# Performance work log

Measured on AMD Instinct MI355X. Metric: run time of the kernel, lower is better.

Reference implementation:

```python
import jax, jax.numpy as jnp
import numpy as np

BS, S, D = 2, 2048, 1024
H = 16
DK = D // H  # 64
ROPE_BASE = 10000.0


def _rope(x):
    # x: [b, s, h, dk]; apply rotary embedding along s with per-pair angles.
    s, d = x.shape[1], x.shape[-1]
    theta = 1.0 / (ROPE_BASE ** (jnp.arange(0, d, 2, dtype=jnp.float32) / d))  # [d/2]
    ang = jnp.arange(s, dtype=jnp.float32)[:, None] * theta[None, :]            # [s, d/2]
    cos = jnp.cos(ang)[None, :, None, :]
    sin = jnp.sin(ang)[None, :, None, :]
    xs = x.reshape(*x.shape[:-1], d // 2, 2)
    x0, x1 = xs[..., 0], xs[..., 1]
    out = jnp.stack([x0 * cos - x1 * sin, x1 * cos + x0 * sin], axis=-1)
    return out.reshape(x.shape)


def setup_inputs() -> dict:
    key = jax.random.key(0)
    ks = jax.random.split(key, 7)
    w = 0.02
    return {
        "Q": jax.random.normal(ks[0], (BS, S, D), dtype=jnp.float32),
        "prev": jax.random.normal(ks[1], (BS, H, S, S), dtype=jnp.float32) * 0.1,
        "Wq": jax.random.normal(ks[2], (D, H * DK), dtype=jnp.float32) * w,
        "bq": jnp.zeros((H * DK,), dtype=jnp.float32),
        "Wk": jax.random.normal(ks[3], (D, H * DK), dtype=jnp.float32) * w,
        "bk": jnp.zeros((H * DK,), dtype=jnp.float32),
        "Wv": jax.random.normal(ks[4], (D, H * DK), dtype=jnp.float32) * w,
        "bv": jnp.zeros((H * DK,), dtype=jnp.float32),
        "Wo": jax.random.normal(ks[5], (H * DK, D), dtype=jnp.float32) * w,
        "bo": jnp.zeros((D,), dtype=jnp.float32),
    }


def reference(Q, prev, Wq, bq, Wk, bk, Wv, bv, Wo, bo):
    bs, s, _ = Q.shape
    scale = DK ** -0.5
    # QKV projections (self-attention: K = V = Q)
    q = (Q @ Wq + bq).reshape(bs, s, H, DK)
    k = (Q @ Wk + bk).reshape(bs, s, H, DK)
    v = (Q @ Wv + bv).reshape(bs, s, H, DK)
    # RoPE on q and k (per-call, matching the torch module)
    q = _rope(q)
    k = _rope(k)
    # scores with residual bias from previous layer
    attn_scores = jnp.einsum("bqhd,bkhd->bhqk", q, k) * scale + prev
    attn_weights = jax.nn.softmax(attn_scores, axis=-1)  # dropout p=0.0
    out = jnp.einsum("bhqk,bkhd->bqhd", attn_weights, v).reshape(bs, s, H * DK)
    out = out @ Wo + bo  # proj dropout p=0.0
    return out, attn_scores
```

## Files before the change

### kernel.cpp

```cpp
#include <hip/hip_runtime.h>
#include <hip/hip_bf16.h>
#include <math.h>

#define S_LEN 2048
#define D_MODEL 1024
#define NH 16
#define DKH 64
#define BSZ 2

typedef __attribute__((ext_vector_type(8))) short s16x8;
typedef __attribute__((ext_vector_type(4))) float f32x4;

__device__ __forceinline__ unsigned short f2bf(float f) {
  unsigned int u = __float_as_uint(f);
  return (unsigned short)((u + 0x7fffu + ((u >> 16) & 1u)) >> 16);
}

__global__ void k_rope_table(float* __restrict__ cosT, float* __restrict__ sinT) {
  int idx = blockIdx.x * 256 + threadIdx.x;
  if (idx >= S_LEN * 32) return;
  int s = idx >> 5, i = idx & 31;
  float theta = powf(10000.0f, -(float)i / 32.0f);
  float ang = (float)s * theta;
  float sv, cv;
  sincosf(ang, &sv, &cv);
  cosT[idx] = cv;
  sinT[idx] = sv;
}

__global__ __launch_bounds__(256) void k_wtrans(const float* __restrict__ W,
                                                unsigned short* __restrict__ WT) {
  __shared__ float t[32][33];
  int n0 = blockIdx.x * 32, k0 = blockIdx.y * 32;
  int tx = threadIdx.x & 31, ty = threadIdx.x >> 5;
#pragma unroll
  for (int p = 0; p < 4; ++p)
    t[ty + p * 8][tx] = W[(size_t)(k0 + ty + p * 8) * 1024 + n0 + tx];
  __syncthreads();
#pragma unroll
  for (int p = 0; p < 4; ++p)
    WT[(size_t)(n0 + ty + p * 8) * 1024 + k0 + tx] = f2bf(t[tx][ty + p * 8]);
}

__global__ __launch_bounds__(256) void k_vtrans(const unsigned short* __restrict__ vl,
                                                unsigned short* __restrict__ vt) {
  __shared__ unsigned short t[64][65];
  int bh = blockIdx.y;
  int s0 = blockIdx.x * 64;
  int tx = threadIdx.x & 3;
  int r = threadIdx.x >> 2;
  const unsigned short* src = vl + (size_t)bh * S_LEN * DKH + (size_t)s0 * DKH;
  s16x8 a = *(const s16x8*)(src + r * 64 + tx * 16);
  s16x8 b = *(const s16x8*)(src + r * 64 + tx * 16 + 8);
#pragma unroll
  for (int j = 0; j < 8; ++j) { t[r][tx * 16 + j] = (unsigned short)a[j]; t[r][tx * 16 + 8 + j] = (unsigned short)b[j]; }
  __syncthreads();
  unsigned short* dst = vt + (size_t)bh * DKH * S_LEN + (size_t)r * S_LEN + s0;
  s16x8 o0, o1;
#pragma unroll
  for (int j = 0; j < 8; ++j) { o0[j] = (short)t[tx * 16 + j][r]; o1[j] = (short)t[tx * 16 + 8 + j][r]; }
  *(s16x8*)(dst + tx * 16) = o0;
  *(s16x8*)(dst + tx * 16 + 8) = o1;
}

__global__ __launch_bounds__(256) void k_qkv(
    const float* __restrict__ Q, const unsigned short* __restrict__ WTqkv,
    const float* __restrict__ bq, const float* __restrict__ bk, const float* __restrict__ bv,
    const float* __restrict__ cosT, const float* __restrict__ sinT,
    unsigned short* __restrict__ ql, unsigned short* __restrict__ kl,
    unsigned short* __restrict__ vl) {
  __shared__ unsigned short As[128][72];
  __shared__ unsigned short Bs[128][72];
  const int m0 = blockIdx.y * 128;
  const int n0 = blockIdx.x * 128;
  const int tid = threadIdx.x;
  const int lane = tid & 63, wave = tid >> 6;
  const int wm = (wave >> 1) * 64, wn = (wave & 1) * 64;
  const int lr = lane & 15, lg = lane >> 4;
  const int widx = n0 >> 10;
  const float* bias = widx == 0 ? bq : (widx == 1 ? bk : bv);

  f32x4 acc[4][4] = {};
  const int arow = tid >> 1, ahalf = tid & 1;

  for (int k0 = 0; k0 < 1024; k0 += 64) {
    __syncthreads();
    {
      const float* src = Q + (size_t)(m0 + arow) * 1024 + k0 + ahalf * 32;
      unsigned short* dstp = &As[arow][ahalf * 32];
#pragma unroll
      for (int j = 0; j < 4; ++j) {
        float4 v0 = ((const float4*)src)[2 * j];
        float4 v1 = ((const float4*)src)[2 * j + 1];
        s16x8 o;
        o[0] = (short)f2bf(v0.x); o[1] = (short)f2bf(v0.y); o[2] = (short)f2bf(v0.z); o[3] = (short)f2bf(v0.w);
        o[4] = (short)f2bf(v1.x); o[5] = (short)f2bf(v1.y); o[6] = (short)f2bf(v1.z); o[7] = (short)f2bf(v1.w);
        *(s16x8*)(dstp + j * 8) = o;
      }
      const s16x8* bsrc = (const s16x8*)(WTqkv + (size_t)(n0 + arow) * 1024 + k0 + ahalf * 32);
      unsigned short* bdst = &Bs[arow][ahalf * 32];
#pragma unroll
      for (int j = 0; j < 4; ++j) *(s16x8*)(bdst + j * 8) = bsrc[j];
    }
    __syncthreads();
#pragma unroll
    for (int ks = 0; ks < 2; ++ks) {
      s16x8 af[4], bf[4];
#pragma unroll
      for (int i = 0; i < 4; ++i) af[i] = *(const s16x8*)&As[wm + i * 16 + lr][ks * 32 + lg * 8];
#pragma unroll
      for (int i = 0; i < 4; ++i) bf[i] = *(const s16x8*)&Bs[wn + i * 16 + lr][ks * 32 + lg * 8];
#pragma unroll
      for (int mi = 0; mi < 4; ++mi)
#pragma unroll
        for (int ni = 0; ni < 4; ++ni)
          acc[mi][ni] = __builtin_amdgcn_mfma_f32_16x16x32_bf16(af[mi], bf[ni], acc[mi][ni], 0, 0, 0);
    }
  }

#pragma unroll
  for (int ni = 0; ni < 4; ++ni) {
    int n = n0 + wn + ni * 16 + lr;
    int np = n & 1023;
    float bval = bias[np];
    int h = np >> 6, d = np & 63;
    int ia = d >> 1;
#pragma unroll
    for (int mi = 0; mi < 4; ++mi) {
#pragma unroll
      for (int r = 0; r < 4; ++r) {
        int m = m0 + wm + mi * 16 + lg * 4 + r;
        int s = m & 2047, b = m >> 11;
        float val = acc[mi][ni][r] + bval;
        size_t oidx = ((size_t)(b * 16 + h) * 2048 + s) * 64 + d;
        if (widx == 2) {
          vl[oidx] = f2bf(val);
        } else {
          float part = __shfl_xor(val, 1);
          float c = cosT[s * 32 + ia], sn = sinT[s * 32 + ia];
          float outv = (d & 1) ? (val * c + part * sn) : (val * c - part * sn);
          (widx == 0 ? ql : kl)[oidx] = f2bf(outv);
        }
      }
    }
  }
}

__global__ __launch_bounds__(256) void k_attn(
    const unsigned short* __restrict__ ql, const unsigned short* __restrict__ kl,
    const unsigned short* __restrict__ vt, const float* __restrict__ prev,
    float* __restrict__ scores, unsigned short* __restrict__ attn_out) {
  __shared__ unsigned short Ks[128][72];
  __shared__ unsigned short Vs[64][136];
  __shared__ unsigned short Ps[4][16][136];
  const int bh = blockIdx.y;
  const int q0 = blockIdx.x * 64;
  const int tid = threadIdx.x, lane = tid & 63, wave = tid >> 6;
  const int lr = lane & 15, lg = lane >> 4;
  const int qw = q0 + wave * 16;

  s16x8 qf[2];
#pragma unroll
  for (int ks = 0; ks < 2; ++ks)
    qf[ks] = *(const s16x8*)(ql + ((size_t)bh * 2048 + qw + lr) * 64 + ks * 32 + lg * 8);

  f32x4 o[4] = {};
  float m_run[4], l_run[4];
#pragma unroll
  for (int r = 0; r < 4; ++r) { m_run[r] = -1e30f; l_run[r] = 0.f; }

  const float scale = 0.125f;
  const float* prevB = prev + (size_t)bh * S_LEN * S_LEN;
  float* scoB = scores + (size_t)bh * S_LEN * S_LEN;

  const int sr = tid >> 1, shf = tid & 1;
  const int dv = tid >> 2, q4 = tid & 3;

  for (int kv0 = 0; kv0 < 2048; kv0 += 128) {
    __syncthreads();
    {
      const s16x8* ksrc = (const s16x8*)(kl + ((size_t)bh * 2048 + kv0 + sr) * 64 + shf * 32);
#pragma unroll
      for (int j = 0; j < 4; ++j) *(s16x8*)&Ks[sr][shf * 32 + j * 8] = ksrc[j];
      const s16x8* vsrc = (const s16x8*)(vt + (size_t)bh * DKH * S_LEN + (size_t)dv * S_LEN + kv0 + q4 * 32);
#pragma unroll
      for (int j = 0; j < 4; ++j) *(s16x8*)&Vs[dv][q4 * 32 + j * 8] = vsrc[j];
    }
    __syncthreads();

    f32x4 sc[8];
#pragma unroll
    for (int n = 0; n < 8; ++n) {
      f32x4 a = {};
#pragma unroll
      for (int ks = 0; ks < 2; ++ks) {
        s16x8 kf = *(const s16x8*)&Ks[n * 16 + lr][ks * 32 + lg * 8];
        a = __builtin_amdgcn_mfma_f32_16x16x32_bf16(qf[ks], kf, a, 0, 0, 0);
      }
      sc[n] = a;
    }

    float tmax[4] = {-1e30f, -1e30f, -1e30f, -1e30f};
#pragma unroll
    for (int n = 0; n < 8; ++n) {
      int col = kv0 + n * 16 + lr;
#pragma unroll
      for (int r = 0; r < 4; ++r) {
        int row = qw + lg * 4 + r;
        float v = sc[n][r] * scale + prevB[(size_t)row * S_LEN + col];
        scoB[(size_t)row * S_LEN + col] = v;
        sc[n][r] = v;
        tmax[r] = fmaxf(tmax[r], v);
      }
    }
#pragma unroll
    for (int mask = 1; mask < 16; mask <<= 1)
#pragma unroll
      for (int r = 0; r < 4; ++r) tmax[r] = fmaxf(tmax[r], __shfl_xor(tmax[r], mask));

    float al[4];
#pragma unroll
    for (int r = 0; r < 4; ++r) {
      float mn = fmaxf(m_run[r], tmax[r]);
      al[r] = __expf(m_run[r] - mn);
      m_run[r] = mn;
      l_run[r] *= al[r];
    }
#pragma unroll
    for (int df = 0; df < 4; ++df)
#pragma unroll
      for (int r = 0; r < 4; ++r) o[df][r] *= al[r];

#pragma unroll
    for (int n = 0; n < 8; ++n) {
#pragma unroll
      for (int r = 0; r < 4; ++r) {
        float p = __expf(sc[n][r] - m_run[r]);
        l_run[r] += p;
        Ps[wave][lg * 4 + r][n * 16 + lr] = f2bf(p);
      }
    }
    __syncthreads();

#pragma unroll
    for (int df = 0; df < 4; ++df) {
#pragma unroll
      for (int ks = 0; ks < 4; ++ks) {
        s16x8 pa = *(const s16x8*)&Ps[wave][lr][ks * 32 + lg * 8];
        s16x8 vb = *(const s16x8*)&Vs[df * 16 + lr][ks * 32 + lg * 8];
        o[df] = __builtin_amdgcn_mfma_f32_16x16x32_bf16(pa, vb, o[df], 0, 0, 0);
      }
    }
  }

#pragma unroll
  for (int mask = 1; mask < 16; mask <<= 1)
#pragma unroll
    for (int r = 0; r < 4; ++r) l_run[r] += __shfl_xor(l_run[r], mask);
  float inv[4];
#pragma unroll
  for (int r = 0; r < 4; ++r) inv[r] = 1.0f / l_run[r];

  int b = bh >> 4, h = bh & 15;
#pragma unroll
  for (int df = 0; df < 4; ++df) {
    int d = df * 16 + lr;
#pragma unroll
    for (int r = 0; r < 4; ++r) {
      int row = qw + lg * 4 + r;
      attn_out[((size_t)(b * 2048 + row)) * 1024 + h * 64 + d] = f2bf(o[df][r] * inv[r]);
    }
  }
}

__global__ __launch_bounds__(256) void k_outproj(
    const unsigned short* __restrict__ A, const unsigned short* __restrict__ WoT,
    const float* __restrict__ bo, float* __restrict__ out) {
  __shared__ unsigned short As[128][72];
  __shared__ unsigned short Bs[128][72];
  const int m0 = blockIdx.y * 128, n0 = blockIdx.x * 128;
  const int tid = threadIdx.x, lane = tid & 63, wave = tid >> 6;
  const int wm = (wave >> 1) * 64, wn = (wave & 1) * 64;
  const int lr = lane & 15, lg = lane >> 4;
  f32x4 acc[4][4] = {};
  const int r = tid >> 1, hfl = tid & 1;
  for (int k0 = 0; k0 < 1024; k0 += 64) {
    __syncthreads();
    const s16x8* asrc = (const s16x8*)(A + (size_t)(m0 + r) * 1024 + k0 + hfl * 32);
    const s16x8* bsrc = (const s16x8*)(WoT + (size_t)(n0 + r) * 1024 + k0 + hfl * 32);
#pragma unroll
    for (int j = 0; j < 4; ++j) {
      *(s16x8*)&As[r][hfl * 32 + j * 8] = asrc[j];
      *(s16x8*)&Bs[r][hfl * 32 + j * 8] = bsrc[j];
    }
    __syncthreads();
#pragma unroll
    for (int ks = 0; ks < 2; ++ks) {
      s16x8 af[4], bf[4];
#pragma unroll
      for (int i = 0; i < 4; ++i) af[i] = *(const s16x8*)&As[wm + i * 16 + lr][ks * 32 + lg * 8];
#pragma unroll
      for (int i = 0; i < 4; ++i) bf[i] = *(const s16x8*)&Bs[wn + i * 16 + lr][ks * 32 + lg * 8];
#pragma unroll
      for (int mi = 0; mi < 4; ++mi)
#pragma unroll
        for (int ni = 0; ni < 4; ++ni)
          acc[mi][ni] = __builtin_amdgcn_mfma_f32_16x16x32_bf16(af[mi], bf[ni], acc[mi][ni], 0, 0, 0);
    }
  }
#pragma unroll
  for (int ni = 0; ni < 4; ++ni) {
    int n = n0 + wn + ni * 16 + lr;
    float bv = bo[n];
#pragma unroll
    for (int mi = 0; mi < 4; ++mi)
#pragma unroll
      for (int rr = 0; rr < 4; ++rr) {
        int m = m0 + wm + mi * 16 + lg * 4 + rr;
        out[(size_t)m * 1024 + n] = acc[mi][ni][rr] + bv;
      }
  }
}

extern "C" void kernel_launch(void* const* d_in, const int* in_sizes, int n_in,
                              void* d_out, int out_size, void* d_ws, size_t ws_size,
                              hipStream_t stream) {
  const float* Q = (const float*)d_in[0];
  const float* prev = (const float*)d_in[1];
  const float* Wq = (const float*)d_in[2];
  const float* bq = (const float*)d_in[3];
  const float* Wk = (const float*)d_in[4];
  const float* bk = (const float*)d_in[5];
  const float* Wv = (const float*)d_in[6];
  const float* bv = (const float*)d_in[7];
  const float* Wo = (const float*)d_in[8];
  const float* bo = (const float*)d_in[9];

  float* out = (float*)d_out;
  float* scores = out + (size_t)4194304;

  char* ws = (char*)d_ws;
  float* cosT = (float*)ws;
  float* sinT = cosT + 65536;
  unsigned short* WTqkv = (unsigned short*)(ws + 524288);
  unsigned short* WoT = WTqkv + 3145728;
  unsigned short* ql = WoT + 1048576;
  unsigned short* kl = ql + 4194304;
  unsigned short* vl = kl + 4194304;
  unsigned short* vt = vl + 4194304;
  unsigned short* attn_out = vt + 4194304;

  k_rope_table<<<256, 256, 0, stream>>>(cosT, sinT);
  k_wtrans<<<dim3(32, 32), 256, 0, stream>>>(Wq, WTqkv);
  k_wtrans<<<dim3(32, 32), 256, 0, stream>>>(Wk, WTqkv + 1048576);
  k_wtrans<<<dim3(32, 32), 256, 0, stream>>>(Wv, WTqkv + 2097152);
  k_wtrans<<<dim3(32, 32), 256, 0, stream>>>(Wo, WoT);
  k_qkv<<<dim3(24, 32), 256, 0, stream>>>(Q, WTqkv, bq, bk, bv, cosT, sinT, ql, kl, vl);
  k_vtrans<<<dim3(32, 32), 256, 0, stream>>>(vl, vt);
  k_attn<<<dim3(32, 32), 256, 0, stream>>>(ql, kl, vt, prev, scores, attn_out);
  k_outproj<<<dim3(8, 32), 256, 0, stream>>>(attn_out, WoT, bo, out);
}
```

Baseline: 410.1 us.

## Rewrite attention with 32x32 MFMA register-resident P and direct global-to-LDS GEMM loads

The attention kernel now computes scores transposed (K as the A operand) with 32x32x16 MFMA. It keeps P in registers via lane shuffles instead of a shared-memory round trip, reads K and V directly from global memory without LDS staging, and uses nontemporal vector loads and stores for prev and scores. The grid is remapped to 512 blocks of 128 queries with launch bounds of 2. The QKV and output projection GEMMs switch to global_load_lds 16-byte async copies into unpadded LDS tiles, and Q is pre-converted to bf16 in a separate kernel. The aim is to cut LDS traffic and syncs and to stream the large fp32 prev/scores arrays efficiently. The risks are more LDS bank conflicts in the unpadded layouts and uncached repeated global reads of K and V.

```diff
diff --git a/kernel.cpp b/kernel.cpp
--- a/kernel.cpp
+++ b/kernel.cpp
@@ -1,19 +1,28 @@
 #include <hip/hip_runtime.h>
 #include <hip/hip_bf16.h>
 #include <math.h>
+#include <cstdint>
 
 #define S_LEN 2048
-#define D_MODEL 1024
-#define NH 16
 #define DKH 64
-#define BSZ 2
 
 typedef __attribute__((ext_vector_type(8))) short s16x8;
+typedef __attribute__((ext_vector_type(4))) short s16x4;
 typedef __attribute__((ext_vector_type(4))) float f32x4;
+typedef __attribute__((ext_vector_type(16))) float f32x16;
 
 __device__ __forceinline__ unsigned short f2bf(float f) {
   unsigned int u = __float_as_uint(f);
   return (unsigned short)((u + 0x7fffu + ((u >> 16) & 1u)) >> 16);
+}
+__device__ __forceinline__ unsigned int pack2bf(float a, float b) {
+  return (unsigned int)f2bf(a) | ((unsigned int)f2bf(b) << 16);
+}
+
+__device__ __forceinline__ void glds16(const unsigned short* g, unsigned short* l) {
+  __builtin_amdgcn_global_load_lds(
+      (const __attribute__((address_space(1))) unsigned int*)(uintptr_t)g,
+      (__attribute__((address_space(3))) unsigned int*)(uintptr_t)l, 16, 0, 0);
 }
 
 __global__ void k_rope_table(float* __restrict__ cosT, float* __restrict__ sinT) {
@@ -42,6 +51,17 @@
     WT[(size_t)(n0 + ty + p * 8) * 1024 + k0 + tx] = f2bf(t[tx][ty + p * 8]);
 }
 
+__global__ __launch_bounds__(256) void k_qconv(const float* __restrict__ Q,
+                                               unsigned short* __restrict__ Qbf) {
+  int idx = (blockIdx.x * 256 + threadIdx.x) * 8;
+  float4 a = *(const float4*)(Q + idx);
+  float4 b = *(const float4*)(Q + idx + 4);
+  s16x8 o;
+  o[0] = (short)f2bf(a.x); o[1] = (short)f2bf(a.y); o[2] = (short)f2bf(a.z); o[3] = (short)f2bf(a.w);
+  o[4] = (short)f2bf(b.x); o[5] = (short)f2bf(b.y); o[6] = (short)f2bf(b.z); o[7] = (short)f2bf(b.w);
+  *(s16x8*)(Qbf + idx) = o;
+}
+
 __global__ __launch_bounds__(256) void k_vtrans(const unsigned short* __restrict__ vl,
                                                 unsigned short* __restrict__ vt) {
   __shared__ unsigned short t[64][65];
@@ -64,52 +84,38 @@
 }
 
 __global__ __launch_bounds__(256) void k_qkv(
-    const float* __restrict__ Q, const unsigned short* __restrict__ WTqkv,
+    const unsigned short* __restrict__ Qbf, const unsigned short* __restrict__ WTqkv,
     const float* __restrict__ bq, const float* __restrict__ bk, const float* __restrict__ bv,
     const float* __restrict__ cosT, const float* __restrict__ sinT,
     unsigned short* __restrict__ ql, unsigned short* __restrict__ kl,
     unsigned short* __restrict__ vl) {
-  __shared__ unsigned short As[128][72];
-  __shared__ unsigned short Bs[128][72];
-  const int m0 = blockIdx.y * 128;
-  const int n0 = blockIdx.x * 128;
-  const int tid = threadIdx.x;
-  const int lane = tid & 63, wave = tid >> 6;
+  __shared__ unsigned short As[128 * 64];
+  __shared__ unsigned short Bs[128 * 64];
+  const int m0 = blockIdx.y * 128, n0 = blockIdx.x * 128;
+  const int tid = threadIdx.x, lane = tid & 63, wave = tid >> 6;
   const int wm = (wave >> 1) * 64, wn = (wave & 1) * 64;
   const int lr = lane & 15, lg = lane >> 4;
   const int widx = n0 >> 10;
   const float* bias = widx == 0 ? bq : (widx == 1 ? bk : bv);
+  const int lrow = lane >> 3, lcol = (lane & 7) * 8;
 
   f32x4 acc[4][4] = {};
-  const int arow = tid >> 1, ahalf = tid & 1;
-
   for (int k0 = 0; k0 < 1024; k0 += 64) {
     __syncthreads();
-    {
-      const float* src = Q + (size_t)(m0 + arow) * 1024 + k0 + ahalf * 32;
-      unsigned short* dstp = &As[arow][ahalf * 32];
-#pragma unroll
-      for (int j = 0; j < 4; ++j) {
-        float4 v0 = ((const float4*)src)[2 * j];
-        float4 v1 = ((const float4*)src)[2 * j + 1];
-        s16x8 o;
-        o[0] = (short)f2bf(v0.x); o[1] = (short)f2bf(v0.y); o[2] = (short)f2bf(v0.z); o[3] = (short)f2bf(v0.w);
-        o[4] = (short)f2bf(v1.x); o[5] = (short)f2bf(v1.y); o[6] = (short)f2bf(v1.z); o[7] = (short)f2bf(v1.w);
-        *(s16x8*)(dstp + j * 8) = o;
-      }
-      const s16x8* bsrc = (const s16x8*)(WTqkv + (size_t)(n0 + arow) * 1024 + k0 + ahalf * 32);
-      unsigned short* bdst = &Bs[arow][ahalf * 32];
-#pragma unroll
-      for (int j = 0; j < 4; ++j) *(s16x8*)(bdst + j * 8) = bsrc[j];
+#pragma unroll
+    for (int i = 0; i < 4; ++i) {
+      int chunk = wave * 4 + i;
+      glds16(Qbf + (size_t)(m0 + 8 * chunk + lrow) * 1024 + k0 + lcol, &As[chunk * 512]);
+      glds16(WTqkv + (size_t)(n0 + 8 * chunk + lrow) * 1024 + k0 + lcol, &Bs[chunk * 512]);
     }
     __syncthreads();
 #pragma unroll
     for (int ks = 0; ks < 2; ++ks) {
       s16x8 af[4], bf[4];
 #pragma unroll
-      for (int i = 0; i < 4; ++i) af[i] = *(const s16x8*)&As[wm + i * 16 + lr][ks * 32 + lg * 8];
-#pragma unroll
-      for (int i = 0; i < 4; ++i) bf[i] = *(const s16x8*)&Bs[wn + i * 16 + lr][ks * 32 + lg * 8];
+      for (int i = 0; i < 4; ++i) af[i] = *(const s16x8*)&As[(wm + i * 16 + lr) * 64 + ks * 32 + lg * 8];
+#pragma unroll
+      for (int i = 0; i < 4; ++i) bf[i] = *(const s16x8*)&Bs[(wn + i * 16 + lr) * 64 + ks * 32 + lg * 8];
 #pragma unroll
       for (int mi = 0; mi < 4; ++mi)
 #pragma unroll
@@ -146,161 +152,167 @@
   }
 }
 
-__global__ __launch_bounds__(256) void k_attn(
+__global__ __launch_bounds__(256, 2) void k_attn(
     const unsigned short* __restrict__ ql, const unsigned short* __restrict__ kl,
     const unsigned short* __restrict__ vt, const float* __restrict__ prev,
     float* __restrict__ scores, unsigned short* __restrict__ attn_out) {
-  __shared__ unsigned short Ks[128][72];
-  __shared__ unsigned short Vs[64][136];
-  __shared__ unsigned short Ps[4][16][136];
-  const int bh = blockIdx.y;
-  const int q0 = blockIdx.x * 64;
+  int wg = blockIdx.x;
+  int c = wg >> 3, r = wg & 7;
+  int bh = r * 4 + (c >> 4);
+  int q0 = (c & 15) * 128;
   const int tid = threadIdx.x, lane = tid & 63, wave = tid >> 6;
-  const int lr = lane & 15, lg = lane >> 4;
-  const int qw = q0 + wave * 16;
-
-  s16x8 qf[2];
-#pragma unroll
-  for (int ks = 0; ks < 2; ++ks)
-    qf[ks] = *(const s16x8*)(ql + ((size_t)bh * 2048 + qw + lr) * 64 + ks * 32 + lg * 8);
-
-  f32x4 o[4] = {};
-  float m_run[4], l_run[4];
-#pragma unroll
-  for (int r = 0; r < 4; ++r) { m_run[r] = -1e30f; l_run[r] = 0.f; }
-
+  const int h = lane >> 5, qcol = lane & 31;
+  const int q = q0 + wave * 32 + qcol;
+
+  const unsigned short* qrow = ql + ((size_t)bh * S_LEN + q) * DKH;
+  s16x8 qf[4];
+#pragma unroll
+  for (int dk = 0; dk < 4; ++dk) qf[dk] = *(const s16x8*)(qrow + dk * 16 + h * 8);
+
+  f32x16 o[2] = {};
+  float m_run = -1e30f, l_run = 0.f;
   const float scale = 0.125f;
-  const float* prevB = prev + (size_t)bh * S_LEN * S_LEN;
-  float* scoB = scores + (size_t)bh * S_LEN * S_LEN;
-
-  const int sr = tid >> 1, shf = tid & 1;
-  const int dv = tid >> 2, q4 = tid & 3;
-
-  for (int kv0 = 0; kv0 < 2048; kv0 += 128) {
-    __syncthreads();
-    {
-      const s16x8* ksrc = (const s16x8*)(kl + ((size_t)bh * 2048 + kv0 + sr) * 64 + shf * 32);
-#pragma unroll
-      for (int j = 0; j < 4; ++j) *(s16x8*)&Ks[sr][shf * 32 + j * 8] = ksrc[j];
-      const s16x8* vsrc = (const s16x8*)(vt + (size_t)bh * DKH * S_LEN + (size_t)dv * S_LEN + kv0 + q4 * 32);
-#pragma unroll
-      for (int j = 0; j < 4; ++j) *(s16x8*)&Vs[dv][q4 * 32 + j * 8] = vsrc[j];
-    }
-    __syncthreads();
-
-    f32x4 sc[8];
-#pragma unroll
-    for (int n = 0; n < 8; ++n) {
-      f32x4 a = {};
-#pragma unroll
-      for (int ks = 0; ks < 2; ++ks) {
-        s16x8 kf = *(const s16x8*)&Ks[n * 16 + lr][ks * 32 + lg * 8];
-        a = __builtin_amdgcn_mfma_f32_16x16x32_bf16(qf[ks], kf, a, 0, 0, 0);
-      }
-      sc[n] = a;
-    }
-
-    float tmax[4] = {-1e30f, -1e30f, -1e30f, -1e30f};
-#pragma unroll
-    for (int n = 0; n < 8; ++n) {
-      int col = kv0 + n * 16 + lr;
-#pragma unroll
-      for (int r = 0; r < 4; ++r) {
-        int row = qw + lg * 4 + r;
-        float v = sc[n][r] * scale + prevB[(size_t)row * S_LEN + col];
-        scoB[(size_t)row * S_LEN + col] = v;
-        sc[n][r] = v;
-        tmax[r] = fmaxf(tmax[r], v);
-      }
-    }
-#pragma unroll
-    for (int mask = 1; mask < 16; mask <<= 1)
-#pragma unroll
-      for (int r = 0; r < 4; ++r) tmax[r] = fmaxf(tmax[r], __shfl_xor(tmax[r], mask));
-
-    float al[4];
-#pragma unroll
-    for (int r = 0; r < 4; ++r) {
-      float mn = fmaxf(m_run[r], tmax[r]);
-      al[r] = __expf(m_run[r] - mn);
-      m_run[r] = mn;
-      l_run[r] *= al[r];
-    }
-#pragma unroll
-    for (int df = 0; df < 4; ++df)
-#pragma unroll
-      for (int r = 0; r < 4; ++r) o[df][r] *= al[r];
-
-#pragma unroll
-    for (int n = 0; n < 8; ++n) {
-#pragma unroll
-      for (int r = 0; r < 4; ++r) {
-        float p = __expf(sc[n][r] - m_run[r]);
-        l_run[r] += p;
-        Ps[wave][lg * 4 + r][n * 16 + lr] = f2bf(p);
-      }
-    }
-    __syncthreads();
-
-#pragma unroll
-    for (int df = 0; df < 4; ++df) {
-#pragma unroll
-      for (int ks = 0; ks < 4; ++ks) {
-        s16x8 pa = *(const s16x8*)&Ps[wave][lr][ks * 32 + lg * 8];
-        s16x8 vb = *(const s16x8*)&Vs[df * 16 + lr][ks * 32 + lg * 8];
-        o[df] = __builtin_amdgcn_mfma_f32_16x16x32_bf16(pa, vb, o[df], 0, 0, 0);
-      }
-    }
-  }
-
-#pragma unroll
-  for (int mask = 1; mask < 16; mask <<= 1)
-#pragma unroll
-    for (int r = 0; r < 4; ++r) l_run[r] += __shfl_xor(l_run[r], mask);
-  float inv[4];
-#pragma unroll
-  for (int r = 0; r < 4; ++r) inv[r] = 1.0f / l_run[r];
-
-  int b = bh >> 4, h = bh & 15;
-#pragma unroll
-  for (int df = 0; df < 4; ++df) {
-    int d = df * 16 + lr;
-#pragma unroll
-    for (int r = 0; r < 4; ++r) {
-      int row = qw + lg * 4 + r;
-      attn_out[((size_t)(b * 2048 + row)) * 1024 + h * 64 + d] = f2bf(o[df][r] * inv[r]);
-    }
-  }
+  const float* prevR = prev + (size_t)bh * S_LEN * S_LEN + (size_t)q * S_LEN;
+  float* scoR = scores + (size_t)bh * S_LEN * S_LEN + (size_t)q * S_LEN;
+  const unsigned short* kbase = kl + (size_t)bh * S_LEN * DKH;
+  const unsigned short* vbase = vt + (size_t)bh * DKH * S_LEN + (size_t)qcol * S_LEN;
+
+  for (int kv0 = 0; kv0 < S_LEN; kv0 += 128) {
+    f32x16 sc[4];
+#pragma unroll
+    for (int t = 0; t < 4; ++t) {
+      const unsigned short* krow = kbase + (size_t)(kv0 + t * 32 + qcol) * DKH + h * 8;
+      f32x16 a = {};
+#pragma unroll
+      for (int dk = 0; dk < 4; ++dk) {
+        s16x8 kf = *(const s16x8*)(krow + dk * 16);
+        a = __builtin_amdgcn_mfma_f32_32x32x16_bf16(kf, qf[dk], a, 0, 0, 0);
+      }
+      sc[t] = a;
+    }
+    float tmax = -1e30f;
+#pragma unroll
+    for (int t = 0; t < 4; ++t) {
+#pragma unroll
+      for (int j = 0; j < 4; ++j) {
+        int kvo = kv0 + t * 32 + 8 * j + 4 * h;
+        f32x4 pv = __builtin_nontemporal_load((const f32x4*)(prevR + kvo));
+        f32x4 sv;
+        sv[0] = sc[t][4 * j + 0] * scale + pv[0];
+        sv[1] = sc[t][4 * j + 1] * scale + pv[1];
+        sv[2] = sc[t][4 * j + 2] * scale + pv[2];
+        sv[3] = sc[t][4 * j + 3] * scale + pv[3];
+        __builtin_nontemporal_store(sv, (f32x4*)(scoR + kvo));
+        sc[t][4 * j + 0] = sv[0]; sc[t][4 * j + 1] = sv[1];
+        sc[t][4 * j + 2] = sv[2]; sc[t][4 * j + 3] = sv[3];
+        tmax = fmaxf(tmax, fmaxf(fmaxf(sv[0], sv[1]), fmaxf(sv[2], sv[3])));
+      }
+    }
+    tmax = fmaxf(tmax, __shfl_xor(tmax, 32));
+    float mn = fmaxf(m_run, tmax);
+    float al = __expf(m_run - mn);
+    m_run = mn;
+    float lsum = 0.f;
+#pragma unroll
+    for (int t = 0; t < 4; ++t)
+#pragma unroll
+      for (int e = 0; e < 16; ++e) {
+        float p = __expf(sc[t][e] - mn);
+        sc[t][e] = p;
+        lsum += p;
+      }
+    l_run = l_run * al + (lsum + __shfl_xor(lsum, 32));
+#pragma unroll
+    for (int dt = 0; dt < 2; ++dt)
+#pragma unroll
+      for (int e = 0; e < 16; ++e) o[dt][e] *= al;
+
+    s16x8 pb[8];
+#pragma unroll
+    for (int g = 0; g < 4; ++g) {
+      unsigned int qu[4][2];
+#pragma unroll
+      for (int j = 0; j < 4; ++j) {
+        qu[j][0] = pack2bf(sc[g][4 * j + 0], sc[g][4 * j + 1]);
+        qu[j][1] = pack2bf(sc[g][4 * j + 2], sc[g][4 * j + 3]);
+      }
+      {
+        unsigned int s0 = h ? qu[0][0] : qu[1][0];
+        unsigned int s1 = h ? qu[0][1] : qu[1][1];
+        unsigned int r0 = __shfl_xor(s0, 32);
+        unsigned int r1 = __shfl_xor(s1, 32);
+        union { s16x8 v; unsigned int u[4]; } fa;
+        fa.u[0] = h ? r0 : qu[0][0];
+        fa.u[1] = h ? r1 : qu[0][1];
+        fa.u[2] = h ? qu[1][0] : r0;
+        fa.u[3] = h ? qu[1][1] : r1;
+        pb[2 * g] = fa.v;
+      }
+      {
+        unsigned int s0 = h ? qu[2][0] : qu[3][0];
+        unsigned int s1 = h ? qu[2][1] : qu[3][1];
+        unsigned int r0 = __shfl_xor(s0, 32);
+        unsigned int r1 = __shfl_xor(s1, 32);
+        union { s16x8 v; unsigned int u[4]; } fb;
+        fb.u[0] = h ? r0 : qu[2][0];
+        fb.u[1] = h ? r1 : qu[2][1];
+        fb.u[2] = h ? qu[3][0] : r0;
+        fb.u[3] = h ? qu[3][1] : r1;
+        pb[2 * g + 1] = fb.v;
+      }
+    }
+#pragma unroll
+    for (int kt = 0; kt < 8; ++kt) {
+      const unsigned short* vrow = vbase + kv0 + kt * 16 + h * 8;
+#pragma unroll
+      for (int dt = 0; dt < 2; ++dt) {
+        s16x8 vf = *(const s16x8*)(vrow + (size_t)dt * 32 * S_LEN);
+        o[dt] = __builtin_amdgcn_mfma_f32_32x32x16_bf16(vf, pb[kt], o[dt], 0, 0, 0);
+      }
+    }
+  }
+
+  float inv = 1.0f / l_run;
+  int b = bh >> 4, hh = bh & 15;
+  unsigned short* orow = attn_out + ((size_t)(b * S_LEN + q)) * 1024 + hh * 64;
+#pragma unroll
+  for (int dt = 0; dt < 2; ++dt)
+#pragma unroll
+    for (int jj = 0; jj < 4; ++jj) {
+      s16x4 ov;
+#pragma unroll
+      for (int i = 0; i < 4; ++i) ov[i] = (short)f2bf(o[dt][4 * jj + i] * inv);
+      *(s16x4*)(orow + dt * 32 + 8 * jj + 4 * h) = ov;
+    }
 }
 
 __global__ __launch_bounds__(256) void k_outproj(
     const unsigned short* __restrict__ A, const unsigned short* __restrict__ WoT,
     const float* __restrict__ bo, float* __restrict__ out) {
-  __shared__ unsigned short As[128][72];
-  __shared__ unsigned short Bs[128][72];
+  __shared__ unsigned short As[128 * 64];
+  __shared__ unsigned short Bs[128 * 64];
   const int m0 = blockIdx.y * 128, n0 = blockIdx.x * 128;
   const int tid = threadIdx.x, lane = tid & 63, wave = tid >> 6;
   const int wm = (wave >> 1) * 64, wn = (wave & 1) * 64;
   const int lr = lane & 15, lg = lane >> 4;
+  const int lrow = lane >> 3, lcol = (lane & 7) * 8;
   f32x4 acc[4][4] = {};
-  const int r = tid >> 1, hfl = tid & 1;
   for (int k0 = 0; k0 < 1024; k0 += 64) {
     __syncthreads();
-    const s16x8* asrc = (const s16x8*)(A + (size_t)(m0 + r) * 1024 + k0 + hfl * 32);
-    const s16x8* bsrc = (const s16x8*)(WoT + (size_t)(n0 + r) * 1024 + k0 + hfl * 32);
-#pragma unroll
-    for (int j = 0; j < 4; ++j) {
-      *(s16x8*)&As[r][hfl * 32 + j * 8] = asrc[j];
-      *(s16x8*)&Bs[r][hfl * 32 + j * 8] = bsrc[j];
+#pragma unroll
+    for (int i = 0; i < 4; ++i) {
+      int chunk = wave * 4 + i;
+      glds16(A + (size_t)(m0 + 8 * chunk + lrow) * 1024 + k0 + lcol, &As[chunk * 512]);
+      glds16(WoT + (size_t)(n0 + 8 * chunk + lrow) * 1024 + k0 + lcol, &Bs[chunk * 512]);
     }
     __syncthreads();
 #pragma unroll
     for (int ks = 0; ks < 2; ++ks) {
       s16x8 af[4], bf[4];
 #pragma unroll
-      for (int i = 0; i < 4; ++i) af[i] = *(const s16x8*)&As[wm + i * 16 + lr][ks * 32 + lg * 8];
-#pragma unroll
-      for (int i = 0; i < 4; ++i) bf[i] = *(const s16x8*)&Bs[wn + i * 16 + lr][ks * 32 + lg * 8];
+      for (int i = 0; i < 4; ++i) af[i] = *(const s16x8*)&As[(wm + i * 16 + lr) * 64 + ks * 32 + lg * 8];
+#pragma unroll
+      for (int i = 0; i < 4; ++i) bf[i] = *(const s16x8*)&Bs[(wn + i * 16 + lr) * 64 + ks * 32 + lg * 8];
 #pragma unroll
       for (int mi = 0; mi < 4; ++mi)
 #pragma unroll
@@ -349,14 +361,16 @@
   unsigned short* vl = kl + 4194304;
   unsigned short* vt = vl + 4194304;
   unsigned short* attn_out = vt + 4194304;
+  unsigned short* Qbf = attn_out + 4194304;
 
   k_rope_table<<<256, 256, 0, stream>>>(cosT, sinT);
   k_wtrans<<<dim3(32, 32), 256, 0, stream>>>(Wq, WTqkv);
   k_wtrans<<<dim3(32, 32), 256, 0, stream>>>(Wk, WTqkv + 1048576);
   k_wtrans<<<dim3(32, 32), 256, 0, stream>>>(Wv, WTqkv + 2097152);
   k_wtrans<<<dim3(32, 32), 256, 0, stream>>>(Wo, WoT);
-  k_qkv<<<dim3(24, 32), 256, 0, stream>>>(Q, WTqkv, bq, bk, bv, cosT, sinT, ql, kl, vl);
+  k_qconv<<<2048, 256, 0, stream>>>(Q, Qbf);
+  k_qkv<<<dim3(24, 32), 256, 0, stream>>>(Qbf, WTqkv, bq, bk, bv, cosT, sinT, ql, kl, vl);
   k_vtrans<<<dim3(32, 32), 256, 0, stream>>>(vl, vt);
-  k_attn<<<dim3(32, 32), 256, 0, stream>>>(ql, kl, vt, prev, scores, attn_out);
+  k_attn<<<512, 256, 0, stream>>>(ql, kl, vt, prev, scores, attn_out);
   k_outproj<<<dim3(8, 32), 256, 0, stream>>>(attn_out, WoT, bo, out);
 }
```

New measurement: 716.4 us. 74.7% more time.

## Use direct global-to-LDS loads, XOR swizzles, bigger attention blocks and XCD-aware mapping

Applied to the files above, without the earlier changes.

Replaces register-staged shared-memory fills in the QKV, attention and output GEMMs with global_load_lds direct copies. This requires a separate kernel that converts Q to bf16 first. The attention kernel moves to 512-thread blocks covering 128 queries, remaps block IDs so heads cluster per XCD, and XOR-swizzles the unpadded K/V/P tiles to avoid bank conflicts. It also drops the barrier before the P·V step, since each wave now uses its own P buffer, and uses nontemporal loads and stores for the large prev/scores streams. The goal is to cut load-issue overhead and cache pollution, at the cost of an extra conversion pass over Q.

```diff
diff --git a/kernel.cpp b/kernel.cpp
--- a/kernel.cpp
+++ b/kernel.cpp
@@ -1,12 +1,10 @@
 #include <hip/hip_runtime.h>
 #include <hip/hip_bf16.h>
 #include <math.h>
+#include <cstdint>
 
 #define S_LEN 2048
-#define D_MODEL 1024
-#define NH 16
 #define DKH 64
-#define BSZ 2
 
 typedef __attribute__((ext_vector_type(8))) short s16x8;
 typedef __attribute__((ext_vector_type(4))) float f32x4;
@@ -14,6 +12,12 @@
 __device__ __forceinline__ unsigned short f2bf(float f) {
   unsigned int u = __float_as_uint(f);
   return (unsigned short)((u + 0x7fffu + ((u >> 16) & 1u)) >> 16);
+}
+
+__device__ __forceinline__ void glds16(const unsigned short* g, unsigned short* l) {
+  __builtin_amdgcn_global_load_lds(
+      (const __attribute__((address_space(1))) unsigned int*)(uintptr_t)g,
+      (__attribute__((address_space(3))) unsigned int*)(uintptr_t)l, 16, 0, 0);
 }
 
 __global__ void k_rope_table(float* __restrict__ cosT, float* __restrict__ sinT) {
@@ -42,6 +46,17 @@
     WT[(size_t)(n0 + ty + p * 8) * 1024 + k0 + tx] = f2bf(t[tx][ty + p * 8]);
 }
 
+__global__ __launch_bounds__(256) void k_qconv(const float* __restrict__ Q,
+                                               unsigned short* __restrict__ Qbf) {
+  int idx = (blockIdx.x * 256 + threadIdx.x) * 8;
+  float4 a = *(const float4*)(Q + idx);
+  float4 b = *(const float4*)(Q + idx + 4);
+  s16x8 o;
+  o[0] = (short)f2bf(a.x); o[1] = (short)f2bf(a.y); o[2] = (short)f2bf(a.z); o[3] = (short)f2bf(a.w);
+  o[4] = (short)f2bf(b.x); o[5] = (short)f2bf(b.y); o[6] = (short)f2bf(b.z); o[7] = (short)f2bf(b.w);
+  *(s16x8*)(Qbf + idx) = o;
+}
+
 __global__ __launch_bounds__(256) void k_vtrans(const unsigned short* __restrict__ vl,
                                                 unsigned short* __restrict__ vt) {
   __shared__ unsigned short t[64][65];
@@ -64,52 +79,38 @@
 }
 
 __global__ __launch_bounds__(256) void k_qkv(
-    const float* __restrict__ Q, const unsigned short* __restrict__ WTqkv,
+    const unsigned short* __restrict__ Qbf, const unsigned short* __restrict__ WTqkv,
     const float* __restrict__ bq, const float* __restrict__ bk, const float* __restrict__ bv,
     const float* __restrict__ cosT, const float* __restrict__ sinT,
     unsigned short* __restrict__ ql, unsigned short* __restrict__ kl,
     unsigned short* __restrict__ vl) {
-  __shared__ unsigned short As[128][72];
-  __shared__ unsigned short Bs[128][72];
-  const int m0 = blockIdx.y * 128;
-  const int n0 = blockIdx.x * 128;
-  const int tid = threadIdx.x;
-  const int lane = tid & 63, wave = tid >> 6;
+  __shared__ unsigned short As[128 * 64];
+  __shared__ unsigned short Bs[128 * 64];
+  const int m0 = blockIdx.y * 128, n0 = blockIdx.x * 128;
+  const int tid = threadIdx.x, lane = tid & 63, wave = tid >> 6;
   const int wm = (wave >> 1) * 64, wn = (wave & 1) * 64;
   const int lr = lane & 15, lg = lane >> 4;
   const int widx = n0 >> 10;
   const float* bias = widx == 0 ? bq : (widx == 1 ? bk : bv);
+  const int lrow = lane >> 3, lcol = (lane & 7) * 8;
 
   f32x4 acc[4][4] = {};
-  const int arow = tid >> 1, ahalf = tid & 1;
-
   for (int k0 = 0; k0 < 1024; k0 += 64) {
     __syncthreads();
-    {
-      const float* src = Q + (size_t)(m0 + arow) * 1024 + k0 + ahalf * 32;
-      unsigned short* dstp = &As[arow][ahalf * 32];
-#pragma unroll
-      for (int j = 0; j < 4; ++j) {
-        float4 v0 = ((const float4*)src)[2 * j];
-        float4 v1 = ((const float4*)src)[2 * j + 1];
-        s16x8 o;
-        o[0] = (short)f2bf(v0.x); o[1] = (short)f2bf(v0.y); o[2] = (short)f2bf(v0.z); o[3] = (short)f2bf(v0.w);
-        o[4] = (short)f2bf(v1.x); o[5] = (short)f2bf(v1.y); o[6] = (short)f2bf(v1.z); o[7] = (short)f2bf(v1.w);
-        *(s16x8*)(dstp + j * 8) = o;
-      }
-      const s16x8* bsrc = (const s16x8*)(WTqkv + (size_t)(n0 + arow) * 1024 + k0 + ahalf * 32);
-      unsigned short* bdst = &Bs[arow][ahalf * 32];
-#pragma unroll
-      for (int j = 0; j < 4; ++j) *(s16x8*)(bdst + j * 8) = bsrc[j];
+#pragma unroll
+    for (int i = 0; i < 4; ++i) {
+      int chunk = wave * 4 + i;
+      glds16(Qbf + (size_t)(m0 + 8 * chunk + lrow) * 1024 + k0 + lcol, &As[chunk * 512]);
+      glds16(WTqkv + (size_t)(n0 + 8 * chunk + lrow) * 1024 + k0 + lcol, &Bs[chunk * 512]);
     }
     __syncthreads();
 #pragma unroll
     for (int ks = 0; ks < 2; ++ks) {
       s16x8 af[4], bf[4];
 #pragma unroll
-      for (int i = 0; i < 4; ++i) af[i] = *(const s16x8*)&As[wm + i * 16 + lr][ks * 32 + lg * 8];
-#pragma unroll
-      for (int i = 0; i < 4; ++i) bf[i] = *(const s16x8*)&Bs[wn + i * 16 + lr][ks * 32 + lg * 8];
+      for (int i = 0; i < 4; ++i) af[i] = *(const s16x8*)&As[(wm + i * 16 + lr) * 64 + ks * 32 + lg * 8];
+#pragma unroll
+      for (int i = 0; i < 4; ++i) bf[i] = *(const s16x8*)&Bs[(wn + i * 16 + lr) * 64 + ks * 32 + lg * 8];
 #pragma unroll
       for (int mi = 0; mi < 4; ++mi)
 #pragma unroll
@@ -146,23 +147,27 @@
   }
 }
 
-__global__ __launch_bounds__(256) void k_attn(
+__global__ __launch_bounds__(512, 4) void k_attn(
     const unsigned short* __restrict__ ql, const unsigned short* __restrict__ kl,
     const unsigned short* __restrict__ vt, const float* __restrict__ prev,
     float* __restrict__ scores, unsigned short* __restrict__ attn_out) {
-  __shared__ unsigned short Ks[128][72];
-  __shared__ unsigned short Vs[64][136];
-  __shared__ unsigned short Ps[4][16][136];
-  const int bh = blockIdx.y;
-  const int q0 = blockIdx.x * 64;
+  __shared__ unsigned short Ks[128 * 64];
+  __shared__ unsigned short Vs[64 * 128];
+  __shared__ unsigned short Ps[8 * 16 * 128];
+
+  int bid = blockIdx.x;
+  int xcd = bid & 7, idx = bid >> 3;
+  int bh = xcd * 4 + (idx >> 4);
+  int qb = idx & 15;
+
   const int tid = threadIdx.x, lane = tid & 63, wave = tid >> 6;
   const int lr = lane & 15, lg = lane >> 4;
-  const int qw = q0 + wave * 16;
+  const int qw = qb * 128 + wave * 16;
 
   s16x8 qf[2];
 #pragma unroll
   for (int ks = 0; ks < 2; ++ks)
-    qf[ks] = *(const s16x8*)(ql + ((size_t)bh * 2048 + qw + lr) * 64 + ks * 32 + lg * 8);
+    qf[ks] = *(const s16x8*)(ql + ((size_t)bh * S_LEN + qw + lr) * DKH + ks * 32 + lg * 8);
 
   f32x4 o[4] = {};
   float m_run[4], l_run[4];
@@ -170,21 +175,28 @@
   for (int r = 0; r < 4; ++r) { m_run[r] = -1e30f; l_run[r] = 0.f; }
 
   const float scale = 0.125f;
+  const unsigned short* kbase = kl + (size_t)bh * S_LEN * DKH;
+  const unsigned short* vbase = vt + (size_t)bh * DKH * S_LEN;
   const float* prevB = prev + (size_t)bh * S_LEN * S_LEN;
   float* scoB = scores + (size_t)bh * S_LEN * S_LEN;
-
-  const int sr = tid >> 1, shf = tid & 1;
-  const int dv = tid >> 2, q4 = tid & 3;
-
-  for (int kv0 = 0; kv0 < 2048; kv0 += 128) {
-    __syncthreads();
-    {
-      const s16x8* ksrc = (const s16x8*)(kl + ((size_t)bh * 2048 + kv0 + sr) * 64 + shf * 32);
-#pragma unroll
-      for (int j = 0; j < 4; ++j) *(s16x8*)&Ks[sr][shf * 32 + j * 8] = ksrc[j];
-      const s16x8* vsrc = (const s16x8*)(vt + (size_t)bh * DKH * S_LEN + (size_t)dv * S_LEN + kv0 + q4 * 32);
-#pragma unroll
-      for (int j = 0; j < 4; ++j) *(s16x8*)&Vs[dv][q4 * 32 + j * 8] = vsrc[j];
+  unsigned short* PsW = &Ps[wave * 2048];
+
+  const int kr = lane >> 3, kc = lane & 7;
+  const int vr = lane >> 4, vc = lane & 15;
+
+  for (int kv0 = 0; kv0 < S_LEN; kv0 += 128) {
+    __syncthreads();
+#pragma unroll
+    for (int half = 0; half < 2; ++half) {
+      int rbase = half * 64 + wave * 8;
+      int row = rbase + kr;
+      glds16(kbase + (size_t)(kv0 + row) * DKH + ((kc ^ (row & 7)) * 8), &Ks[rbase * 64]);
+    }
+#pragma unroll
+    for (int half = 0; half < 2; ++half) {
+      int dbase = wave * 8 + half * 4;
+      int d = dbase + vr;
+      glds16(vbase + (size_t)d * S_LEN + kv0 + ((vc ^ (d & 7)) * 8), &Vs[dbase * 128]);
     }
     __syncthreads();
 
@@ -194,7 +206,9 @@
       f32x4 a = {};
 #pragma unroll
       for (int ks = 0; ks < 2; ++ks) {
-        s16x8 kf = *(const s16x8*)&Ks[n * 16 + lr][ks * 32 + lg * 8];
+        int row = n * 16 + lr;
+        s16x8 kf = *(const s16x8*)((const char*)Ks +
+                                   row * 128 + ((ks * 64 + lg * 16) ^ ((lr & 7) << 4)));
         a = __builtin_amdgcn_mfma_f32_16x16x32_bf16(qf[ks], kf, a, 0, 0, 0);
       }
       sc[n] = a;
@@ -207,8 +221,9 @@
 #pragma unroll
       for (int r = 0; r < 4; ++r) {
         int row = qw + lg * 4 + r;
-        float v = sc[n][r] * scale + prevB[(size_t)row * S_LEN + col];
-        scoB[(size_t)row * S_LEN + col] = v;
+        float pv = __builtin_nontemporal_load(prevB + (size_t)row * S_LEN + col);
+        float v = sc[n][r] * scale + pv;
+        __builtin_nontemporal_store(v, scoB + (size_t)row * S_LEN + col);
         sc[n][r] = v;
         tmax[r] = fmaxf(tmax[r], v);
       }
@@ -237,17 +252,21 @@
       for (int r = 0; r < 4; ++r) {
         float p = __expf(sc[n][r] - m_run[r]);
         l_run[r] += p;
-        Ps[wave][lg * 4 + r][n * 16 + lr] = f2bf(p);
-      }
-    }
-    __syncthreads();
+        int prow = lg * 4 + r;
+        *(unsigned short*)((char*)PsW + prow * 256 +
+                           ((n * 32 + lr * 2) ^ ((prow & 7) << 4))) = f2bf(p);
+      }
+    }
 
 #pragma unroll
     for (int df = 0; df < 4; ++df) {
 #pragma unroll
       for (int ks = 0; ks < 4; ++ks) {
-        s16x8 pa = *(const s16x8*)&Ps[wave][lr][ks * 32 + lg * 8];
-        s16x8 vb = *(const s16x8*)&Vs[df * 16 + lr][ks * 32 + lg * 8];
+        s16x8 pa = *(const s16x8*)((const char*)PsW +
+                                   lr * 256 + ((ks * 64 + lg * 16) ^ ((lr & 7) << 4)));
+        int vrow = df * 16 + lr;
+        s16x8 vb = *(const s16x8*)((const char*)Vs +
+                                   vrow * 256 + ((ks * 64 + lg * 16) ^ ((lr & 7) << 4)));
         o[df] = __builtin_amdgcn_mfma_f32_16x16x32_bf16(pa, vb, o[df], 0, 0, 0);
       }
     }
@@ -268,7 +287,7 @@
 #pragma unroll
     for (int r = 0; r < 4; ++r) {
       int row = qw + lg * 4 + r;
-      attn_out[((size_t)(b * 2048 + row)) * 1024 + h * 64 + d] = f2bf(o[df][r] * inv[r]);
+      attn_out[((size_t)(b * S_LEN + row)) * 1024 + h * 64 + d] = f2bf(o[df][r] * inv[r]);
     }
   }
 }
@@ -276,31 +295,30 @@
 __global__ __launch_bounds__(256) void k_outproj(
     const unsigned short* __restrict__ A, const unsigned short* __restrict__ WoT,
     const float* __restrict__ bo, float* __restrict__ out) {
-  __shared__ unsigned short As[128][72];
-  __shared__ unsigned short Bs[128][72];
+  __shared__ unsigned short As[128 * 64];
+  __shared__ unsigned short Bs[128 * 64];
   const int m0 = blockIdx.y * 128, n0 = blockIdx.x * 128;
   const int tid = threadIdx.x, lane = tid & 63, wave = tid >> 6;
   const int wm = (wave >> 1) * 64, wn = (wave & 1) * 64;
   const int lr = lane & 15, lg = lane >> 4;
+  const int lrow = lane >> 3, lcol = (lane & 7) * 8;
   f32x4 acc[4][4] = {};
-  const int r = tid >> 1, hfl = tid & 1;
   for (int k0 = 0; k0 < 1024; k0 += 64) {
     __syncthreads();
-    const s16x8* asrc = (const s16x8*)(A + (size_t)(m0 + r) * 1024 + k0 + hfl * 32);
-    const s16x8* bsrc = (const s16x8*)(WoT + (size_t)(n0 + r) * 1024 + k0 + hfl * 32);
-#pragma unroll
-    for (int j = 0; j < 4; ++j) {
-      *(s16x8*)&As[r][hfl * 32 + j * 8] = asrc[j];
-      *(s16x8*)&Bs[r][hfl * 32 + j * 8] = bsrc[j];
+#pragma unroll
+    for (int i = 0; i < 4; ++i) {
+      int chunk = wave * 4 + i;
+      glds16(A + (size_t)(m0 + 8 * chunk + lrow) * 1024 + k0 + lcol, &As[chunk * 512]);
+      glds16(WoT + (size_t)(n0 + 8 * chunk + lrow) * 1024 + k0 + lcol, &Bs[chunk * 512]);
     }
     __syncthreads();
 #pragma unroll
     for (int ks = 0; ks < 2; ++ks) {
       s16x8 af[4], bf[4];
 #pragma unroll
-      for (int i = 0; i < 4; ++i) af[i] = *(const s16x8*)&As[wm + i * 16 + lr][ks * 32 + lg * 8];
-#pragma unroll
-      for (int i = 0; i < 4; ++i) bf[i] = *(const s16x8*)&Bs[wn + i * 16 + lr][ks * 32 + lg * 8];
+      for (int i = 0; i < 4; ++i) af[i] = *(const s16x8*)&As[(wm + i * 16 + lr) * 64 + ks * 32 + lg * 8];
+#pragma unroll
+      for (int i = 0; i < 4; ++i) bf[i] = *(const s16x8*)&Bs[(wn + i * 16 + lr) * 64 + ks * 32 + lg * 8];
 #pragma unroll
       for (int mi = 0; mi < 4; ++mi)
 #pragma unroll
@@ -349,14 +367,16 @@
   unsigned short* vl = kl + 4194304;
   unsigned short* vt = vl + 4194304;
   unsigned short* attn_out = vt + 4194304;
+  unsigned short* Qbf = attn_out + 4194304;
 
   k_rope_table<<<256, 256, 0, stream>>>(cosT, sinT);
   k_wtrans<<<dim3(32, 32), 256, 0, stream>>>(Wq, WTqkv);
   k_wtrans<<<dim3(32, 32), 256, 0, stream>>>(Wk, WTqkv + 1048576);
   k_wtrans<<<dim3(32, 32), 256, 0, stream>>>(Wv, WTqkv + 2097152);
   k_wtrans<<<dim3(32, 32), 256, 0, stream>>>(Wo, WoT);
-  k_qkv<<<dim3(24, 32), 256, 0, stream>>>(Q, WTqkv, bq, bk, bv, cosT, sinT, ql, kl, vl);
+  k_qconv<<<2048, 256, 0, stream>>>(Q, Qbf);
+  k_qkv<<<dim3(24, 32), 256, 0, stream>>>(Qbf, WTqkv, bq, bk, bv, cosT, sinT, ql, kl, vl);
   k_vtrans<<<dim3(32, 32), 256, 0, stream>>>(vl, vt);
-  k_attn<<<dim3(32, 32), 256, 0, stream>>>(ql, kl, vt, prev, scores, attn_out);
+  k_attn<<<512, 512, 0, stream>>>(ql, kl, vt, prev, scores, attn_out);
   k_outproj<<<dim3(8, 32), 256, 0, stream>>>(attn_out, WoT, bo, out);
 }
```

Result: slower. 526.1 us (+28.3%).
